# Performance work log

Measured on AMD Instinct MI355X. Metric: run time of the kernel, lower is better.

The kernel has to match this reference:

```python
import jax, jax.numpy as jnp
import numpy as np

B, N, C, H, WS, SS = 16, 4096, 512, 8, 8, 4
HD = C // H
SCALE = HD ** -0.5
NW = N // WS  # number of mask windows (= 512)
B_ = B * NW   # windows-times-batch after the view(-1, WS, C)


def _make_mask():
    # faithful replication of create_mask(), including the non-standard
    # window_partition (reshape->transpose->reshape) used by the repo
    img = np.zeros(N, dtype=np.float32)
    img[N - WS:N - SS] = 1.0
    img[N - SS:] = 2.0
    # window_partition on (1, N, 1) then .view(-1, WS):
    mw = img.reshape(N // WS, WS).T.reshape(N // WS, WS)  # (NW, WS)
    am = mw[:, None, :] - mw[:, :, None]                   # (NW, WS, WS)
    return jnp.asarray(np.where(am != 0.0, -100.0, 0.0).astype(np.float32))

ATTN_MASK = _make_mask()  # (NW, WS, WS)


def _layernorm(x, w, b, eps=1e-5):
    mu = jnp.mean(x, axis=-1, keepdims=True)
    var = jnp.mean((x - mu) ** 2, axis=-1, keepdims=True)
    return (x - mu) * jax.lax.rsqrt(var + eps) * w + b


def setup_inputs() -> dict:
    key = jax.random.key(0)
    ks = jax.random.split(key, 8)
    s = 0.02
    return {
        'x': jax.random.normal(ks[0], (B, N, C), jnp.float32),
        'norm1_w': jnp.ones((C,), jnp.float32),
        'norm1_b': jnp.zeros((C,), jnp.float32),
        'qkv_w': jax.random.normal(ks[1], (C, 3 * C), jnp.float32) * s,
        'qkv_b': jnp.zeros((3 * C,), jnp.float32),
        'proj_w': jax.random.normal(ks[2], (C, C), jnp.float32) * s,
        'proj_b': jnp.zeros((C,), jnp.float32),
        'norm2_w': jnp.ones((C,), jnp.float32),
        'norm2_b': jnp.zeros((C,), jnp.float32),
        'mlp_w1': jax.random.normal(ks[3], (C, 4 * C), jnp.float32) * s,
        'mlp_b1': jnp.zeros((4 * C,), jnp.float32),
        'mlp_w2': jax.random.normal(ks[4], (4 * C, C), jnp.float32) * s,
        'mlp_b2': jnp.zeros((C,), jnp.float32),
    }


def reference(x, norm1_w, norm1_b, qkv_w, qkv_b, proj_w, proj_b,
              norm2_w, norm2_b, mlp_w1, mlp_b1, mlp_w2, mlp_b2):
    shortcut = x
    h = _layernorm(x, norm1_w, norm1_b)
    h = jnp.roll(h, -SS, axis=1)  # shift_size > 0
    # repo's window_partition: (B,N,C) -> (B, N//WS, WS, C) -> perm -> (B*WS, N//WS, C)
    win = h.reshape(B, N // WS, WS, C).transpose(0, 2, 1, 3)
    # then .view(-1, WS, C): reinterpret flat buffer as (B_, WS, C)
    win = win.reshape(B_, WS, C)
    qkv = (win @ qkv_w + qkv_b).reshape(B_, WS, 3, H, HD).transpose(2, 0, 3, 1, 4)
    q, k, v = qkv[0], qkv[1], qkv[2]              # (B_, H, WS, HD)
    attn = jnp.einsum('bhqd,bhkd->bhqk', q, k) * SCALE
    attn = attn.reshape(B, NW, H, WS, WS) + ATTN_MASK[None, :, None]
    attn = jax.nn.softmax(attn.reshape(B_, H, WS, WS), axis=-1)
    out = jnp.einsum('bhqk,bhkd->bqhd', attn, v).reshape(B_, WS, C)
    out = out @ proj_w + proj_b
    # repo's window_reverse on the (B_, WS, C) buffer
    out = out.reshape(B, N // WS, WS, C).transpose(0, 2, 1, 3).reshape(B, N, C)
    out = jnp.roll(out, SS, axis=1)
    x = shortcut + out
    h2 = _layernorm(x, norm2_w, norm2_b)
    h2 = jax.nn.gelu(h2 @ mlp_w1 + mlp_b1, approximate=False)
    return x + (h2 @ mlp_w2 + mlp_b2)
```

## Files before the change

kernel.cpp:

```cpp
#include <hip/hip_runtime.h>
#include <hip/hip_bf16.h>
#include <cstdint>
#include <cstddef>

typedef __hip_bfloat16 BF16;
typedef __bf16 bf16x8 __attribute__((ext_vector_type(8)));
typedef float floatx4 __attribute__((ext_vector_type(4)));

static constexpr size_t OFF_WQKV  = 0;
static constexpr size_t OFF_WPROJ = OFF_WQKV  + (size_t)1536 * 512 * 2;
static constexpr size_t OFF_W1    = OFF_WPROJ + (size_t)512 * 512 * 2;
static constexpr size_t OFF_W2    = OFF_W1    + (size_t)2048 * 512 * 2;
static constexpr size_t OFF_H     = OFF_W2    + (size_t)512 * 2048 * 2;
static constexpr size_t OFF_QKV   = OFF_H     + (size_t)65536 * 512 * 2;
static constexpr size_t OFF_ATTN  = OFF_QKV   + (size_t)65536 * 1536 * 2;
static constexpr size_t OFF_M     = OFF_QKV;

__global__ __launch_bounds__(256) void prep_ln_kernel(
    const float* __restrict__ qkvw, const float* __restrict__ projw,
    const float* __restrict__ w1, const float* __restrict__ w2,
    BF16* __restrict__ o_qkv, BF16* __restrict__ o_proj,
    BF16* __restrict__ o_w1, BF16* __restrict__ o_w2,
    const float* __restrict__ x, const float* __restrict__ n1w,
    const float* __restrict__ n1b, BF16* __restrict__ hbuf) {
  __shared__ float t[64][65];
  const int tid = threadIdx.x;
  if (blockIdx.x < 768) {
    int b = blockIdx.x;
    const float* W; BF16* Wt; int K, N, bx, by;
    if (b < 192)      {          W = qkvw;  Wt = o_qkv;  K = 512;  N = 1536; bx = b % 24; by = b / 24; }
    else if (b < 256) { b -= 192; W = projw; Wt = o_proj; K = 512;  N = 512;  bx = b % 8;  by = b / 8; }
    else if (b < 512) { b -= 256; W = w1;    Wt = o_w1;   K = 512;  N = 2048; bx = b % 32; by = b / 32; }
    else              { b -= 512; W = w2;    Wt = o_w2;   K = 2048; N = 512;  bx = b % 8;  by = b / 8; }
    const int n0 = bx * 64, k0 = by * 64;
#pragma unroll
    for (int it = 0; it < 16; ++it) {
      int idx = it * 256 + tid;
      int r = idx >> 6, c = idx & 63;
      t[r][c] = W[(size_t)(k0 + r) * N + (n0 + c)];
    }
    __syncthreads();
#pragma unroll
    for (int it = 0; it < 16; ++it) {
      int idx = it * 256 + tid;
      int r = idx >> 6, c = idx & 63;
      Wt[(size_t)(n0 + r) * K + (k0 + c)] = __float2bfloat16(t[c][r]);
    }
  } else {
    const int lane = tid & 63;
    const size_t row = (size_t)(blockIdx.x - 768) * 4 + (tid >> 6);
    const float* xr = x + row * 512 + lane * 8;
    float xv[8], wv[8], bv[8];
    *(float4*)&xv[0] = *(const float4*)xr;
    *(float4*)&xv[4] = *(const float4*)(xr + 4);
    *(float4*)&wv[0] = *(const float4*)(n1w + lane * 8);
    *(float4*)&wv[4] = *(const float4*)(n1w + lane * 8 + 4);
    *(float4*)&bv[0] = *(const float4*)(n1b + lane * 8);
    *(float4*)&bv[4] = *(const float4*)(n1b + lane * 8 + 4);
    float s = 0.0f, ss = 0.0f;
#pragma unroll
    for (int tt = 0; tt < 8; ++tt) { s += xv[tt]; ss += xv[tt] * xv[tt]; }
#pragma unroll
    for (int o = 32; o > 0; o >>= 1) { s += __shfl_xor(s, o); ss += __shfl_xor(ss, o); }
    const float mu = s * (1.0f / 512.0f);
    const float var = ss * (1.0f / 512.0f) - mu * mu;
    const float rs = rsqrtf(var + 1e-5f);
    BF16 ob[8];
#pragma unroll
    for (int tt = 0; tt < 8; ++tt)
      ob[tt] = __float2bfloat16((xv[tt] - mu) * rs * wv[tt] + bv[tt]);
    *(uint4*)(hbuf + row * 512 + lane * 8) = *(const uint4*)ob;
  }
}

__global__ __launch_bounds__(256) void ln_kernel(
    const float* __restrict__ x, const float* __restrict__ w,
    const float* __restrict__ b, BF16* __restrict__ out) {
  const int lane = threadIdx.x & 63;
  const size_t row = (size_t)blockIdx.x * 4 + (threadIdx.x >> 6);
  const float* xr = x + row * 512 + lane * 8;
  float xv[8], wv[8], bv[8];
  *(float4*)&xv[0] = *(const float4*)xr;
  *(float4*)&xv[4] = *(const float4*)(xr + 4);
  *(float4*)&wv[0] = *(const float4*)(w + lane * 8);
  *(float4*)&wv[4] = *(const float4*)(w + lane * 8 + 4);
  *(float4*)&bv[0] = *(const float4*)(b + lane * 8);
  *(float4*)&bv[4] = *(const float4*)(b + lane * 8 + 4);
  float s = 0.0f, ss = 0.0f;
#pragma unroll
  for (int t = 0; t < 8; ++t) { s += xv[t]; ss += xv[t] * xv[t]; }
#pragma unroll
  for (int o = 32; o > 0; o >>= 1) { s += __shfl_xor(s, o); ss += __shfl_xor(ss, o); }
  const float mu = s * (1.0f / 512.0f);
  const float var = ss * (1.0f / 512.0f) - mu * mu;
  const float rs = rsqrtf(var + 1e-5f);
  BF16 ob[8];
#pragma unroll
  for (int t = 0; t < 8; ++t)
    ob[t] = __float2bfloat16((xv[t] - mu) * rs * wv[t] + bv[t]);
  *(uint4*)(out + row * 512 + lane * 8) = *(const uint4*)ob;
}

__device__ __forceinline__ void gload16(const BF16* g, const char* l) {
  __builtin_amdgcn_global_load_lds(
      (const __attribute__((address_space(1))) void*)g,
      (__attribute__((address_space(3))) void*)l, 16, 0, 0);
}

__device__ __forceinline__ int win_src_row(int r) {
  const int b = r >> 12;
  const int s = (r >> 9) & 7;
  const int mm = (r >> 3) & 63;
  const int j = r & 7;
  const int p = (64 * mm + 8 * j + s + 4) & 4095;
  return (b << 12) + p;
}

__device__ __forceinline__ float fast_gelu(float v) {
  const float t = __expf(v * -1.702f);
  return v * __builtin_amdgcn_rcpf(1.0f + t);
}

__device__ __forceinline__ uint2 pack4bf(float a, float b, float c, float d) {
  union { BF16 h[4]; uint2 u; } u;
  u.h[0] = __float2bfloat16(a); u.h[1] = __float2bfloat16(b);
  u.h[2] = __float2bfloat16(c); u.h[3] = __float2bfloat16(d);
  return u.u;
}

#define GATE4 asm volatile("s_waitcnt vmcnt(4)" ::: "memory")
#define GATE2 asm volatile("s_waitcnt vmcnt(2)" ::: "memory")
#define GATE0 asm volatile("s_waitcnt vmcnt(0)" ::: "memory")
#define BAR() __builtin_amdgcn_s_barrier()
#define WAITL() asm volatile("s_waitcnt lgkmcnt(0)" ::: "memory")

template <int ROWMAP, int EPI, int K>
__global__ __launch_bounds__(512, 2) void gemm256(
    const BF16* __restrict__ A, const BF16* __restrict__ Bt,
    const float* __restrict__ bias, const float* __restrict__ resid,
    float* __restrict__ outf, BF16* __restrict__ outb, int Nout) {
  __shared__ __align__(16) char smem[131072];
  const int tid = threadIdx.x, lane = tid & 63, wv = tid >> 6;
  const int wm = wv >> 2, wn = wv & 3;

  const int gx = gridDim.x;
  const int nwg = gx * gridDim.y;
  const int hwid = blockIdx.y * gx + blockIdx.x;
  const int swz = (hwid & 7) * (nwg >> 3) + (hwid >> 3);
  const int bm = swz / gx, bn = swz - bm * gx;
  const int row0 = bm * 256, col0 = bn * 256;

  const int srow = lane >> 3;
  const int scol = ((lane & 7) ^ srow) * 8;
  const BF16* Pa[2][2];
  const BF16* Pb[2][2];
#pragma unroll
  for (int mh = 0; mh < 2; ++mh)
#pragma unroll
    for (int c = 0; c < 2; ++c) {
      int ra = row0 + mh * 128 + c * 64 + wv * 8 + srow;
      if (ROWMAP == 1) ra = win_src_row(ra);
      Pa[mh][c] = A + (size_t)ra * K + scol;
      const int rb = col0 + mh * 128 + c * 64 + wv * 8 + srow;
      Pb[mh][c] = Bt + (size_t)rb * K + scol;
    }
  const int ldsw = wv * 1024;

  const int r16 = lane & 15;
  const int sx0 = (((lane >> 4) + 0) ^ (r16 & 7)) * 16;
  const int sx1 = (((lane >> 4) + 4) ^ (r16 & 7)) * 16;
  const int raby = (wm * 64 + r16) * 128;
  const int rbby = (wn * 32 + r16) * 128;

  floatx4 acc[2][4][2][2];
#pragma unroll
  for (int mh = 0; mh < 2; ++mh)
#pragma unroll
    for (int m2 = 0; m2 < 4; ++m2)
#pragma unroll
      for (int nh = 0; nh < 2; ++nh)
#pragma unroll
        for (int n2 = 0; n2 < 2; ++n2)
          acc[mh][m2][nh][n2] = floatx4{0.f, 0.f, 0.f, 0.f};

  bf16x8 fa[4][2], fb0[2][2], fb1[2][2];

#define STG_A(half, dd) do {                                              \
    gload16(Pa[half][0], smem + (dd)*65536 + (half)*16384 + ldsw);        \
    gload16(Pa[half][1], smem + (dd)*65536 + (half)*16384 + 8192 + ldsw); \
  } while (0)
#define STG_B(half, dd) do {                                                      \
    gload16(Pb[half][0], smem + (dd)*65536 + 32768 + (half)*16384 + ldsw);        \
    gload16(Pb[half][1], smem + (dd)*65536 + 32768 + (half)*16384 + 8192 + ldsw); \
  } while (0)
#define ADV() do {                                          \
    Pa[0][0] += 64; Pa[0][1] += 64; Pa[1][0] += 64; Pa[1][1] += 64; \
    Pb[0][0] += 64; Pb[0][1] += 64; Pb[1][0] += 64; Pb[1][1] += 64; \
  } while (0)

#define RD_FA(mh, dd)                                                          \
  _Pragma("unroll")                                                            \
  for (int m2 = 0; m2 < 4; ++m2) {                                             \
    fa[m2][0] = *(const bf16x8*)(smem + (dd)*65536 + (mh)*16384 + raby + m2*2048 + sx0); \
    fa[m2][1] = *(const bf16x8*)(smem + (dd)*65536 + (mh)*16384 + raby + m2*2048 + sx1); \
  }
#define RD_FB(dst, nh, dd)                                                     \
  _Pragma("unroll")                                                            \
  for (int n2 = 0; n2 < 2; ++n2) {                                             \
    dst[n2][0] = *(const bf16x8*)(smem + (dd)*65536 + 32768 + (nh)*16384 + rbby + n2*2048 + sx0); \
    dst[n2][1] = *(const bf16x8*)(smem + (dd)*65536 + 32768 + (nh)*16384 + rbby + n2*2048 + sx1); \
  }
#define MF(mh, nh, fbx)                                                        \
  __builtin_amdgcn_s_setprio(1);                                               \
  _Pragma("unroll")                                                            \
  for (int ks = 0; ks < 2; ++ks)                                               \
    _Pragma("unroll")                                                          \
    for (int m2 = 0; m2 < 4; ++m2)                                             \
      _Pragma("unroll")                                                        \
      for (int n2 = 0; n2 < 2; ++n2)                                           \
        acc[mh][m2][nh][n2] = __builtin_amdgcn_mfma_f32_16x16x32_bf16(         \
            fbx[n2][ks], fa[m2][ks], acc[mh][m2][nh][n2], 0, 0, 0);            \
  __builtin_amdgcn_s_setprio(0)

  STG_A(0, 0);
  STG_B(0, 0);
  STG_B(1, 0);
  STG_A(1, 0);
  ADV();
  GATE4;
  BAR();

  constexpr int NT = K / 64;
  for (int t = 0; t < NT - 1; ++t) {
    const int dd = t & 1, de = dd ^ 1;
    RD_FA(0, dd); RD_FB(fb0, 0, dd);
    STG_A(0, de);
    WAITL();
    MF(0, 0, fb0);
    GATE4; BAR();
    RD_FB(fb1, 1, dd);
    STG_B(0, de);
    WAITL();
    MF(0, 1, fb1);
    GATE4; BAR();
    RD_FA(1, dd);
    STG_B(1, de);
    WAITL();
    MF(1, 1, fb1);
    BAR();
    STG_A(1, de);
    MF(1, 0, fb0);
    GATE4; BAR();
    ADV();
  }
  {
    const int dd = (NT - 1) & 1;
    RD_FA(0, dd); RD_FB(fb0, 0, dd);
    WAITL();
    MF(0, 0, fb0);
    GATE2; BAR();
    RD_FB(fb1, 1, dd);
    WAITL();
    MF(0, 1, fb1);
    GATE0; BAR();
    RD_FA(1, dd);
    WAITL();
    MF(1, 1, fb1);
    MF(1, 0, fb0);
  }
#undef STG_A
#undef STG_B
#undef ADV
#undef RD_FA
#undef RD_FB
#undef MF

  const int g4 = (lane >> 4) * 4;
  float4 bsv[2][2];
#pragma unroll
  for (int nh = 0; nh < 2; ++nh)
#pragma unroll
    for (int n2 = 0; n2 < 2; ++n2)
      bsv[nh][n2] = *(const float4*)&bias[col0 + nh * 128 + wn * 32 + n2 * 16 + g4];

#pragma unroll
  for (int mh = 0; mh < 2; ++mh)
#pragma unroll
    for (int m2 = 0; m2 < 4; ++m2) {
      const int r = row0 + mh * 128 + wm * 64 + m2 * 16 + r16;
      size_t rowbase;
      if (EPI == 2) {
        const int b = r >> 12;
        const int np = (r >> 3) & 511;
        const int ap = r & 7;
        const int io = ((ap << 9) + np + 4) & 4095;
        rowbase = ((size_t)(b << 12) + io) * 512;
      } else {
        rowbase = (size_t)r * Nout;
      }
#pragma unroll
      for (int nh = 0; nh < 2; ++nh)
#pragma unroll
        for (int n2 = 0; n2 < 2; ++n2) {
          const int c0 = col0 + nh * 128 + wn * 32 + n2 * 16 + g4;
          floatx4 v = acc[mh][m2][nh][n2];
          v[0] += bsv[nh][n2].x; v[1] += bsv[nh][n2].y;
          v[2] += bsv[nh][n2].z; v[3] += bsv[nh][n2].w;
          if (EPI == 0) {
            *(uint2*)&outb[rowbase + c0] = pack4bf(v[0], v[1], v[2], v[3]);
          } else if (EPI == 1) {
            *(uint2*)&outb[rowbase + c0] = pack4bf(
                fast_gelu(v[0]), fast_gelu(v[1]), fast_gelu(v[2]), fast_gelu(v[3]));
          } else if (EPI == 2) {
            const float4 rv = *(const float4*)&resid[rowbase + c0];
            float4 ov = {rv.x + v[0], rv.y + v[1], rv.z + v[2], rv.w + v[3]};
            *(float4*)&outf[rowbase + c0] = ov;
          } else {
            float4 ov = *(float4*)&outf[rowbase + c0];
            ov.x += v[0]; ov.y += v[1]; ov.z += v[2]; ov.w += v[3];
            *(float4*)&outf[rowbase + c0] = ov;
          }
        }
    }
}

__global__ __launch_bounds__(64) void attn_kernel(
    const BF16* __restrict__ qkv, BF16* __restrict__ out) {
  const int w = blockIdx.x;
  const int lane = threadIdx.x;
  const int qi = lane >> 3, kj = lane & 7;
  __shared__ __align__(16) BF16 sm[8 * 1544];
  const BF16* src = qkv + (size_t)w * 8 * 1536;
#pragma unroll
  for (int rr = 0; rr < 8; ++rr) {
    const uint4* s4 = (const uint4*)(src + (size_t)rr * 1536);
    uint4* d4 = (uint4*)(&sm[rr * 1544]);
#pragma unroll
    for (int c = 0; c < 3; ++c) d4[c * 64 + lane] = s4[c * 64 + lane];
  }
  __syncthreads();

  const int s = (w >> 6) & 7, mm = w & 63;
  const int pi = 64 * mm + 8 * qi + s;
  const int pj = 64 * mm + 8 * kj + s;
  const int ri = pi >= 4092 ? 2 : (pi >= 4088 ? 1 : 0);
  const int rj = pj >= 4092 ? 2 : (pj >= 4088 ? 1 : 0);
  const float maskv = (ri != rj) ? -100.0f : 0.0f;

  for (int h = 0; h < 8; ++h) {
    const BF16* qp = &sm[qi * 1544 + h * 64];
    const BF16* kp = &sm[kj * 1544 + 512 + h * 64];
    float acc = 0.0f;
#pragma unroll
    for (int d0 = 0; d0 < 8; ++d0) {
      bf16x8 qv = *(const bf16x8*)(qp + d0 * 8);
      bf16x8 kv = *(const bf16x8*)(kp + d0 * 8);
#pragma unroll
      for (int t = 0; t < 8; ++t) acc += (float)qv[t] * (float)kv[t];
    }
    float sc = acc * 0.125f + maskv;
    float mx = sc;
    mx = fmaxf(mx, __shfl_xor(mx, 1, 8));
    mx = fmaxf(mx, __shfl_xor(mx, 2, 8));
    mx = fmaxf(mx, __shfl_xor(mx, 4, 8));
    float e = __expf(sc - mx);
    float den = e;
    den += __shfl_xor(den, 1, 8);
    den += __shfl_xor(den, 2, 8);
    den += __shfl_xor(den, 4, 8);
    const float P = e / den;

    float o8[8];
#pragma unroll
    for (int t = 0; t < 8; ++t) o8[t] = 0.0f;
#pragma unroll
    for (int j2 = 0; j2 < 8; ++j2) {
      float p2 = __shfl(P, j2, 8);
      bf16x8 vv = *(const bf16x8*)(&sm[j2 * 1544 + 1024 + h * 64 + kj * 8]);
#pragma unroll
      for (int t = 0; t < 8; ++t) o8[t] += p2 * (float)vv[t];
    }
    BF16 ob[8];
#pragma unroll
    for (int t = 0; t < 8; ++t) ob[t] = __float2bfloat16(o8[t]);
    *(uint4*)(&out[((size_t)w * 8 + qi) * 512 + h * 64 + kj * 8]) = *(const uint4*)ob;
  }
}

extern "C" void kernel_launch(void* const* d_in, const int* in_sizes, int n_in,
                              void* d_out, int out_size, void* d_ws, size_t ws_size,
                              hipStream_t stream) {
  (void)in_sizes; (void)n_in; (void)out_size; (void)ws_size;
  const float* x     = (const float*)d_in[0];
  const float* n1w   = (const float*)d_in[1];
  const float* n1b   = (const float*)d_in[2];
  const float* qkvw  = (const float*)d_in[3];
  const float* qkvb  = (const float*)d_in[4];
  const float* projw = (const float*)d_in[5];
  const float* projb = (const float*)d_in[6];
  const float* n2w   = (const float*)d_in[7];
  const float* n2b   = (const float*)d_in[8];
  const float* w1    = (const float*)d_in[9];
  const float* b1    = (const float*)d_in[10];
  const float* w2    = (const float*)d_in[11];
  const float* b2    = (const float*)d_in[12];
  float* out = (float*)d_out;
  char* ws = (char*)d_ws;

  BF16* wt_qkv  = (BF16*)(ws + OFF_WQKV);
  BF16* wt_proj = (BF16*)(ws + OFF_WPROJ);
  BF16* wt_w1   = (BF16*)(ws + OFF_W1);
  BF16* wt_w2   = (BF16*)(ws + OFF_W2);
  BF16* hbuf    = (BF16*)(ws + OFF_H);
  BF16* qkvbuf  = (BF16*)(ws + OFF_QKV);
  BF16* attnbuf = (BF16*)(ws + OFF_ATTN);
  BF16* mbuf    = (BF16*)(ws + OFF_M);

  prep_ln_kernel<<<768 + 16384, 256, 0, stream>>>(
      qkvw, projw, w1, w2, wt_qkv, wt_proj, wt_w1, wt_w2,
      x, n1w, n1b, hbuf);

  gemm256<1, 0, 512><<<dim3(6, 256), 512, 0, stream>>>(hbuf, wt_qkv, qkvb, nullptr, nullptr, qkvbuf, 1536);
  attn_kernel<<<8192, 64, 0, stream>>>(qkvbuf, attnbuf);
  gemm256<0, 2, 512><<<dim3(2, 256), 512, 0, stream>>>(attnbuf, wt_proj, projb, x, out, nullptr, 512);
  ln_kernel<<<16384, 256, 0, stream>>>(out, n2w, n2b, hbuf);
  gemm256<0, 1, 512><<<dim3(8, 256), 512, 0, stream>>>(hbuf, wt_w1, b1, nullptr, nullptr, mbuf, 2048);
  gemm256<0, 3, 2048><<<dim3(2, 256), 512, 0, stream>>>(mbuf, wt_w2, b2, nullptr, out, nullptr, 512);
}
```

Measured before the change: 687.9 us.

## Restructure GEMM main loop into two-stage unrolled pipeline with deeper prefetch

Rewrites the GEMM K-loop so each iteration handles two K-tiles, with fixed LDS buffers and explicit k offsets in place of pointer advancing. Quarter-tiles of the next buffer are prefetched earlier, so two quarter-tiles of the second stage are in flight before the loop starts. This aims to hide global-load latency better and drop the separate epilogue iteration. In exchange it adds barriers around every LDS read phase. It also assumes NT is even and that the staggered buffer reuse is correctly ordered, which is a race risk.

```diff
diff --git a/kernel.cpp b/kernel.cpp
--- a/kernel.cpp
+++ b/kernel.cpp
@@ -129,7 +129,6 @@
 }
 
 #define GATE4 asm volatile("s_waitcnt vmcnt(4)" ::: "memory")
-#define GATE2 asm volatile("s_waitcnt vmcnt(2)" ::: "memory")
 #define GATE0 asm volatile("s_waitcnt vmcnt(0)" ::: "memory")
 #define BAR() __builtin_amdgcn_s_barrier()
 #define WAITL() asm volatile("s_waitcnt lgkmcnt(0)" ::: "memory")
@@ -185,17 +184,13 @@
 
   bf16x8 fa[4][2], fb0[2][2], fb1[2][2];
 
-#define STG_A(half, dd) do {                                              \
-    gload16(Pa[half][0], smem + (dd)*65536 + (half)*16384 + ldsw);        \
-    gload16(Pa[half][1], smem + (dd)*65536 + (half)*16384 + 8192 + ldsw); \
+#define STG_A_K(half, dd, koff) do {                                            \
+    gload16(Pa[half][0] + (koff), smem + (dd)*65536 + (half)*16384 + ldsw);     \
+    gload16(Pa[half][1] + (koff), smem + (dd)*65536 + (half)*16384 + 8192 + ldsw); \
   } while (0)
-#define STG_B(half, dd) do {                                                      \
-    gload16(Pb[half][0], smem + (dd)*65536 + 32768 + (half)*16384 + ldsw);        \
-    gload16(Pb[half][1], smem + (dd)*65536 + 32768 + (half)*16384 + 8192 + ldsw); \
-  } while (0)
-#define ADV() do {                                          \
-    Pa[0][0] += 64; Pa[0][1] += 64; Pa[1][0] += 64; Pa[1][1] += 64; \
-    Pb[0][0] += 64; Pb[0][1] += 64; Pb[1][0] += 64; Pb[1][1] += 64; \
+#define STG_B_K(half, dd, koff) do {                                                    \
+    gload16(Pb[half][0] + (koff), smem + (dd)*65536 + 32768 + (half)*16384 + ldsw);     \
+    gload16(Pb[half][1] + (koff), smem + (dd)*65536 + 32768 + (half)*16384 + 8192 + ldsw); \
   } while (0)
 
 #define RD_FA(mh, dd)                                                          \
@@ -222,55 +217,62 @@
             fbx[n2][ks], fa[m2][ks], acc[mh][m2][nh][n2], 0, 0, 0);            \
   __builtin_amdgcn_s_setprio(0)
 
-  STG_A(0, 0);
-  STG_B(0, 0);
-  STG_B(1, 0);
-  STG_A(1, 0);
-  ADV();
+  STG_A_K(0, 0, 0);
+  STG_B_K(0, 0, 0);
+  STG_B_K(1, 0, 0);
+  STG_A_K(1, 0, 0);
+  STG_A_K(0, 1, 64);
+  STG_B_K(1, 1, 64);
   GATE4;
   BAR();
 
   constexpr int NT = K / 64;
-  for (int t = 0; t < NT - 1; ++t) {
-    const int dd = t & 1, de = dd ^ 1;
-    RD_FA(0, dd); RD_FB(fb0, 0, dd);
-    STG_A(0, de);
-    WAITL();
+  constexpr int NI = NT / 2;
+  for (int i = 0; i < NI; ++i) {
+    const bool last = (i == NI - 1);
+    const int k1 = (2 * i + 1) * 64;
+    const int k2 = k1 + 64, k3 = k1 + 128;
+    RD_FA(0, 0); RD_FB(fb0, 0, 0);
+    STG_B_K(0, 1, k1);
+    BAR(); WAITL();
     MF(0, 0, fb0);
-    GATE4; BAR();
-    RD_FB(fb1, 1, dd);
-    STG_B(0, de);
-    WAITL();
+    BAR();
+    RD_FB(fb1, 1, 0);
+    STG_A_K(1, 1, k1);
+    BAR(); WAITL();
     MF(0, 1, fb1);
-    GATE4; BAR();
-    RD_FA(1, dd);
-    STG_B(1, de);
-    WAITL();
+    BAR();
+    RD_FA(1, 0);
+    if (!last) STG_A_K(0, 0, k2);
+    BAR(); WAITL();
     MF(1, 1, fb1);
     BAR();
-    STG_A(1, de);
+    if (!last) STG_B_K(1, 0, k2);
     MF(1, 0, fb0);
-    GATE4; BAR();
-    ADV();
-  }
-  {
-    const int dd = (NT - 1) & 1;
-    RD_FA(0, dd); RD_FB(fb0, 0, dd);
-    WAITL();
+    if (!last) { GATE4; } else { GATE0; }
+    BAR();
+    RD_FA(0, 1); RD_FB(fb0, 0, 1);
+    if (!last) STG_B_K(0, 0, k2);
+    BAR(); WAITL();
     MF(0, 0, fb0);
-    GATE2; BAR();
-    RD_FB(fb1, 1, dd);
-    WAITL();
+    BAR();
+    RD_FB(fb1, 1, 1);
+    if (!last) STG_A_K(1, 0, k2);
+    BAR(); WAITL();
     MF(0, 1, fb1);
-    GATE0; BAR();
-    RD_FA(1, dd);
-    WAITL();
+    BAR();
+    RD_FA(1, 1);
+    if (!last) STG_A_K(0, 1, k3);
+    BAR(); WAITL();
     MF(1, 1, fb1);
+    BAR();
+    if (!last) STG_B_K(1, 1, k3);
     MF(1, 0, fb0);
-  }
-#undef STG_A
-#undef STG_B
-#undef ADV
+    if (!last) GATE4;
+    BAR();
+  }
+#undef STG_A_K
+#undef STG_B_K
 #undef RD_FA
 #undef RD_FB
 #undef MF
```

Result: slower. 727.1 us (+5.7%).
